# Kernel optimization log

Measured on AMD Instinct MI355X. Metric: run time of the kernel, lower is better.

## Reference

```python
import jax, jax.numpy as jnp
import numpy as np

N = 50000   # nodes
E = 800000  # edges (avg degree 16)
D = 128     # in_feats == out_feats


def setup_inputs() -> dict:
    key = jax.random.key(0)
    k1, k2, k3, k4 = jax.random.split(key, 4)
    h = jax.random.normal(k1, (N, D), dtype=jnp.float32)
    src = jax.random.randint(k2, (E,), 0, N, dtype=jnp.int32)
    dst = jax.random.randint(k3, (E,), 0, N, dtype=jnp.int32)
    snorm_n = jnp.ones((N, 1), dtype=jnp.float32)  # sqrt(1/N) replicated; identity-scaled here
    # NodeApply linear: Linear(2*D, D) with bias
    W = jax.random.normal(k4, (D, 2 * D), dtype=jnp.float32) / np.sqrt(2 * D).astype(np.float32)
    b = jnp.zeros((D,), dtype=jnp.float32)
    return {"h": h, "snorm_n": snorm_n, "W": W, "b": b, "src": src, "dst": dst}


def reference(h, snorm_n, W, b, src, dst):
    # dropout p=0.0 -> identity
    h_in = h
    # gather neighbor messages and segment-mean aggregate (MeanAggregator)
    ones = jnp.ones((src.shape[0],), dtype=h.dtype)
    deg = jax.ops.segment_sum(ones, dst, num_segments=N)            # [N]
    msg_sum = jax.ops.segment_sum(h[src], dst, num_segments=N)     # [N, D]
    c = msg_sum / jnp.maximum(deg, 1.0)[:, None]                   # zero-degree nodes -> c = 0
    # NodeApply: concat -> linear -> L2 normalize -> relu
    bundle = jnp.concatenate([h, c], axis=1) @ W.T + b             # [N, D]
    nrm = jnp.sqrt(jnp.sum(bundle * bundle, axis=1, keepdims=True))
    bundle = bundle / jnp.maximum(nrm, 1e-12)                      # F.normalize(p=2, dim=1)
    out = jax.nn.relu(bundle)
    # graph norm
    out = out * snorm_n
    # residual (in_feats == out_feats)
    return h_in + out
```

## Files before the change

### kernel.cpp

```cpp
#include <hip/hip_runtime.h>
#include <hip/hip_bf16.h>

#define TPB 256
#define CHUNK_LOG 13
#define CHUNK (1 << CHUNK_LOG)
#define HSTRIDE 12544

typedef __attribute__((ext_vector_type(8))) short bf16x8;
typedef __attribute__((ext_vector_type(4))) float f32x4;
typedef __attribute__((ext_vector_type(2))) float f32x2;

__device__ inline unsigned short f2bf(float f) {
    unsigned u = __float_as_uint(f);
    unsigned r = u + 0x7fffu + ((u >> 16) & 1u);
    return (unsigned short)(r >> 16);
}
__device__ inline float bf2f(unsigned short s) {
    return __uint_as_float(((unsigned)s) << 16);
}

__global__ void k_hist(const int* __restrict__ dst,
                       unsigned* __restrict__ hist32, unsigned char* __restrict__ lrank,
                       unsigned* ctr, int E) {
    __shared__ unsigned lhist[HSTRIDE];
    int b = blockIdx.x;
    if (b == 0 && threadIdx.x == 0) *ctr = 0u;
    for (int i = threadIdx.x; i < HSTRIDE; i += TPB) lhist[i] = 0;
    __syncthreads();
    int e0 = b << CHUNK_LOG;
    int e1 = min(e0 + CHUNK, E);
    for (int e = e0 + (int)threadIdx.x; e < e1; e += TPB) {
        int d = dst[e];
        unsigned sh = (d & 3) * 8;
        unsigned old = atomicAdd(&lhist[d >> 2], 1u << sh);
        lrank[e] = (unsigned char)((old >> sh) & 0xffu);
    }
    __syncthreads();
    for (int i = threadIdx.x; i < HSTRIDE; i += TPB)
        hist32[(size_t)b * HSTRIDE + i] = lhist[i];
}

__launch_bounds__(TPB)
__global__ void k_scan(const unsigned* __restrict__ hist32,
                       unsigned short* __restrict__ cbase,
                       int* __restrict__ bsum, unsigned* ctr,
                       int* __restrict__ offs, int N, int E, int NBH) {
    extern __shared__ unsigned tile[];
    __shared__ int sdata[4];
    __shared__ int sb[TPB];
    __shared__ int wsum[4];
    int NB = gridDim.x;
    int bid = blockIdx.x, tid = threadIdx.x;
    int lane = tid & 63, w = tid >> 6;

    int tileBase = bid * 64;
    int total = NBH * 64;
    for (int i = tid; i < total; i += TPB) {
        int b = i >> 6, c = i & 63;
        tile[i] = hist32[(size_t)b * HSTRIDE + tileBase + c];
    }
    __syncthreads();
    int n = bid * TPB + tid;
    unsigned sh = (tid & 3) * 8;
    int wcol = tid >> 2;
    int run = 0;
    for (int b = 0; b < NBH; ++b) {
        int c = (int)((tile[b * 64 + wcol] >> sh) & 0xffu);
        if (n < N) cbase[(size_t)b * N + n] = (unsigned short)run;
        run += c;
    }
    int dv = (n < N) ? run : 0;

    int s = dv;
    for (int o = 32; o; o >>= 1) s += __shfl_xor(s, o);
    if (lane == 0) sdata[w] = s;
    __syncthreads();
    if (tid == 0) {
        int tot = sdata[0] + sdata[1] + sdata[2] + sdata[3];
        __hip_atomic_store(&bsum[bid], tot, __ATOMIC_RELAXED, __HIP_MEMORY_SCOPE_AGENT);
        __hip_atomic_fetch_add(ctr, 1u, __ATOMIC_RELEASE, __HIP_MEMORY_SCOPE_AGENT);
        while (__hip_atomic_load(ctr, __ATOMIC_ACQUIRE, __HIP_MEMORY_SCOPE_AGENT)
               < (unsigned)NB)
            __builtin_amdgcn_s_sleep(2);
    }
    __syncthreads();

    int v = 0;
    if (tid < NB)
        v = __hip_atomic_load(&bsum[tid], __ATOMIC_RELAXED, __HIP_MEMORY_SCOPE_AGENT);
    int x = v;
    for (int o = 1; o < 64; o <<= 1) { int y = __shfl_up(x, o); if (lane >= o) x += y; }
    if (lane == 63) wsum[w] = x;
    __syncthreads();
    int add = 0;
    for (int k = 0; k < w; ++k) add += wsum[k];
    sb[tid] = add + x - v;
    __syncthreads();
    int base = sb[bid];

    int y2 = dv;
    for (int o = 1; o < 64; o <<= 1) { int z = __shfl_up(y2, o); if (lane >= o) y2 += z; }
    __syncthreads();
    if (lane == 63) wsum[w] = y2;
    __syncthreads();
    int add2 = 0;
    for (int k = 0; k < w; ++k) add2 += wsum[k];
    int ex = base + add2 + y2 - dv;
    if (n < N) offs[n] = ex;
    if (n == N - 1) offs[N] = E;
}

__global__ void k_scatterconv(const float* __restrict__ h, const float* __restrict__ W,
                              const int* __restrict__ src, const int* __restrict__ dst,
                              const unsigned char* __restrict__ lrank,
                              const unsigned short* __restrict__ cbase,
                              const int* __restrict__ offs,
                              unsigned short* __restrict__ esrc,
                              unsigned short* __restrict__ h_hi,
                              unsigned* __restrict__ h8,
                              unsigned short* __restrict__ Wb,
                              int N, int E, int nchunk) {
    int nh4 = N * 32;
    int totalc = nh4 + 8192;
    for (int t = blockIdx.x * TPB + threadIdx.x; t < totalc; t += gridDim.x * TPB) {
        if (t < nh4) {
            float4 v = ((const float4*)h)[t];
            ushort4 hi;
            hi.x = f2bf(v.x); hi.y = f2bf(v.y);
            hi.z = f2bf(v.z); hi.w = f2bf(v.w);
            ((ushort4*)h_hi)[t] = hi;
            int p8 = __builtin_amdgcn_cvt_pk_fp8_f32(v.x, v.y, 0, false);
            p8 = __builtin_amdgcn_cvt_pk_fp8_f32(v.z, v.w, p8, true);
            h8[t] = (unsigned)p8;
        } else {
            int w4 = t - nh4;
            float4 v = ((const float4*)W)[w4];
            ushort4 hi;
            hi.x = f2bf(v.x); hi.y = f2bf(v.y);
            hi.z = f2bf(v.z); hi.w = f2bf(v.w);
            ((ushort4*)Wb)[w4] = hi;
        }
    }
    int slice = blockIdx.x & 7;
    int chunk = blockIdx.x >> 3;
    int lo = (int)((long long)N * slice >> 3);
    int hi = (int)((long long)N * (slice + 1) >> 3);
    for (int e = chunk * TPB + threadIdx.x; e < E; e += nchunk * TPB) {
        int d = dst[e];
        if (d >= lo && d < hi) {
            int b = e >> CHUNK_LOG;
            int pos = offs[d] + (int)cbase[(size_t)b * N + d] + (int)lrank[e];
            esrc[pos] = (unsigned short)src[e];
        }
    }
}

#define AGG_ACC(u)                                                            \
    {                                                                         \
        f32x2 _p = __builtin_amdgcn_cvt_pk_f32_fp8((int)(u), false);          \
        f32x2 _q = __builtin_amdgcn_cvt_pk_f32_fp8((int)(u), true);           \
        a0 += _p.x; a1 += _p.y; a2 += _q.x; a3 += _q.y;                       \
    }

__global__ void k_agg(const unsigned* __restrict__ h8, const int* __restrict__ offs,
                      const unsigned short* __restrict__ esrc,
                      unsigned* __restrict__ c8, int N) {
    int wav = (blockIdx.x * TPB + threadIdx.x) >> 6;
    int half = (threadIdx.x >> 5) & 1;
    int hl = threadIdx.x & 31;
    int n = wav * 2 + half;
    if (n >= N) return;
    int beg = offs[n], end = offs[n + 1];
    int cnt = end - beg;
    float a0 = 0.f, a1 = 0.f, a2 = 0.f, a3 = 0.f;
    int e = beg;
    int s0 = 0, s1 = 0, s2 = 0, s3 = 0, s4 = 0, s5 = 0, s6 = 0, s7 = 0;
    if (cnt >= 8) {
        s0 = esrc[e];     s1 = esrc[e + 1]; s2 = esrc[e + 2]; s3 = esrc[e + 3];
        s4 = esrc[e + 4]; s5 = esrc[e + 5]; s6 = esrc[e + 6]; s7 = esrc[e + 7];
    }
    while (cnt >= 16) {
        int t0 = esrc[e + 8],  t1 = esrc[e + 9],  t2 = esrc[e + 10], t3 = esrc[e + 11];
        int t4 = esrc[e + 12], t5 = esrc[e + 13], t6 = esrc[e + 14], t7 = esrc[e + 15];
        unsigned u0 = h8[(size_t)s0 * 32 + hl];
        unsigned u1 = h8[(size_t)s1 * 32 + hl];
        unsigned u2 = h8[(size_t)s2 * 32 + hl];
        unsigned u3 = h8[(size_t)s3 * 32 + hl];
        unsigned u4 = h8[(size_t)s4 * 32 + hl];
        unsigned u5 = h8[(size_t)s5 * 32 + hl];
        unsigned u6 = h8[(size_t)s6 * 32 + hl];
        unsigned u7 = h8[(size_t)s7 * 32 + hl];
        AGG_ACC(u0) AGG_ACC(u1) AGG_ACC(u2) AGG_ACC(u3)
        AGG_ACC(u4) AGG_ACC(u5) AGG_ACC(u6) AGG_ACC(u7)
        s0 = t0; s1 = t1; s2 = t2; s3 = t3;
        s4 = t4; s5 = t5; s6 = t6; s7 = t7;
        e += 8; cnt -= 8;
    }
    if (cnt >= 8) {
        unsigned u0 = h8[(size_t)s0 * 32 + hl];
        unsigned u1 = h8[(size_t)s1 * 32 + hl];
        unsigned u2 = h8[(size_t)s2 * 32 + hl];
        unsigned u3 = h8[(size_t)s3 * 32 + hl];
        unsigned u4 = h8[(size_t)s4 * 32 + hl];
        unsigned u5 = h8[(size_t)s5 * 32 + hl];
        unsigned u6 = h8[(size_t)s6 * 32 + hl];
        unsigned u7 = h8[(size_t)s7 * 32 + hl];
        AGG_ACC(u0) AGG_ACC(u1) AGG_ACC(u2) AGG_ACC(u3)
        AGG_ACC(u4) AGG_ACC(u5) AGG_ACC(u6) AGG_ACC(u7)
        e += 8; cnt -= 8;
    }
    for (; cnt > 0; --cnt, ++e) {
        unsigned u0 = h8[(size_t)esrc[e] * 32 + hl];
        AGG_ACC(u0)
    }
    float inv = 1.0f / fmaxf((float)(end - beg), 1.0f);
    int pk = __builtin_amdgcn_cvt_pk_fp8_f32(a0 * inv, a1 * inv, 0, false);
    pk = __builtin_amdgcn_cvt_pk_fp8_f32(a2 * inv, a3 * inv, pk, true);
    c8[(size_t)n * 32 + hl] = (unsigned)pk;
}

__launch_bounds__(TPB)
__global__ void k_apply(const unsigned short* __restrict__ h_hi,
                        const unsigned char* __restrict__ c8,
                        const unsigned short* __restrict__ Wb,
                        const float* __restrict__ bia,
                        const float* __restrict__ snorm,
                        float* __restrict__ out, int N) {
    int lane = threadIdx.x & 63;
    int l15 = lane & 15, l4 = lane >> 4;
    int wave = threadIdx.x >> 6;
    int r0 = blockIdx.x * 128 + wave * 32;

    f32x4 acc[2][8] = {};

    #pragma unroll
    for (int kc = 0; kc < 8; ++kc) {
        bf16x8 Bf[8];
        #pragma unroll
        for (int n = 0; n < 8; ++n) {
            Bf[n] = *(const bf16x8*)((const char*)Wb +
                     ((size_t)(n * 16 + l15) * 512 + (size_t)kc * 64 + (size_t)l4 * 16));
        }
        #pragma unroll
        for (int rf = 0; rf < 2; ++rf) {
            int row = r0 + rf * 16 + l15;
            if (row > N - 1) row = N - 1;
            bf16x8 av;
            if (kc < 4) {
                av = *(const bf16x8*)((const char*)h_hi +
                      ((size_t)row * 256 + (size_t)kc * 64 + (size_t)l4 * 16));
            } else {
                uint2 cu = *(const uint2*)(c8 + (size_t)row * 128 +
                            (size_t)(kc - 4) * 32 + (size_t)l4 * 8);
                f32x2 p = __builtin_amdgcn_cvt_pk_f32_fp8((int)cu.x, false);
                f32x2 q = __builtin_amdgcn_cvt_pk_f32_fp8((int)cu.x, true);
                f32x2 r = __builtin_amdgcn_cvt_pk_f32_fp8((int)cu.y, false);
                f32x2 s = __builtin_amdgcn_cvt_pk_f32_fp8((int)cu.y, true);
                union { unsigned u[4]; bf16x8 v; } cv;
                asm("v_cvt_pk_bf16_f32 %0, %1, %2" : "=v"(cv.u[0]) : "v"(p.x), "v"(p.y));
                asm("v_cvt_pk_bf16_f32 %0, %1, %2" : "=v"(cv.u[1]) : "v"(q.x), "v"(q.y));
                asm("v_cvt_pk_bf16_f32 %0, %1, %2" : "=v"(cv.u[2]) : "v"(r.x), "v"(r.y));
                asm("v_cvt_pk_bf16_f32 %0, %1, %2" : "=v"(cv.u[3]) : "v"(s.x), "v"(s.y));
                av = cv.v;
            }
            #pragma unroll
            for (int n = 0; n < 8; ++n)
                acc[rf][n] = __builtin_amdgcn_mfma_f32_16x16x32_bf16(av, Bf[n], acc[rf][n], 0, 0, 0);
        }
    }

    float bn[8];
    #pragma unroll
    for (int n = 0; n < 8; ++n) bn[n] = bia[n * 16 + l15];

    #pragma unroll
    for (int rf = 0; rf < 2; ++rf) {
        float sq[4] = {0.f, 0.f, 0.f, 0.f};
        #pragma unroll
        for (int n = 0; n < 8; ++n) {
            #pragma unroll
            for (int g = 0; g < 4; ++g) {
                acc[rf][n][g] += bn[n];
                sq[g] += acc[rf][n][g] * acc[rf][n][g];
            }
        }
        #pragma unroll
        for (int g = 0; g < 4; ++g) {
            sq[g] += __shfl_xor(sq[g], 1);
            sq[g] += __shfl_xor(sq[g], 2);
            sq[g] += __shfl_xor(sq[g], 4);
            sq[g] += __shfl_xor(sq[g], 8);
        }
        #pragma unroll
        for (int g = 0; g < 4; ++g) {
            int row = r0 + rf * 16 + l4 * 4 + g;
            if (row < N) {
                float invn = 1.0f / fmaxf(sqrtf(sq[g]), 1e-12f);
                float sn = snorm[row];
                #pragma unroll
                for (int n = 0; n < 8; ++n) {
                    int col = n * 16 + l15;
                    float res = bf2f(h_hi[(size_t)row * 128 + col]);
                    float v = fmaxf(acc[rf][n][g] * invn, 0.f) * sn + res;
                    __builtin_nontemporal_store(v, &out[(size_t)row * 128 + col]);
                }
            }
        }
    }
}

extern "C" void kernel_launch(void* const* d_in, const int* in_sizes, int n_in,
                              void* d_out, int out_size, void* d_ws, size_t ws_size,
                              hipStream_t stream) {
    const float* h     = (const float*)d_in[0];
    const float* snorm = (const float*)d_in[1];
    const float* W     = (const float*)d_in[2];
    const float* b     = (const float*)d_in[3];
    const int*   src   = (const int*)d_in[4];
    const int*   dst   = (const int*)d_in[5];
    int N = in_sizes[1];
    int E = in_sizes[4];
    float* out = (float*)d_out;

    char* ws = (char*)d_ws;
    size_t off = 0;
    auto alloc = [&](size_t bytes) {
        void* ptr = ws + off;
        off = (off + bytes + 255) & ~(size_t)255;
        return ptr;
    };
    int NB  = (N + TPB - 1) / TPB;
    int NBH = (E + CHUNK - 1) >> CHUNK_LOG;
    int* offs   = (int*)alloc((size_t)(N + 1) * 4);
    int* bsum   = (int*)alloc((size_t)NB * 4);
    unsigned* ctr          = (unsigned*)alloc(256);
    unsigned* hist32       = (unsigned*)alloc((size_t)NBH * HSTRIDE * 4);
    unsigned short* cbase  = (unsigned short*)alloc((size_t)NBH * N * 2);
    unsigned char*  lrank  = (unsigned char*)alloc((size_t)E);
    unsigned short* esrc   = (unsigned short*)alloc((size_t)E * 2);
    unsigned short* h_hi   = (unsigned short*)alloc((size_t)N * 128 * 2);
    unsigned*       h8     = (unsigned*)alloc((size_t)N * 128);
    unsigned short* Wb     = (unsigned short*)alloc((size_t)128 * 256 * 2);
    unsigned* c8 = hist32;

    k_hist<<<NBH, TPB, 0, stream>>>(dst, hist32, lrank, ctr, E);

    size_t tile_bytes = (size_t)NBH * 64 * 4;
    k_scan<<<NB, TPB, tile_bytes, stream>>>(hist32, cbase, bsum, ctr, offs, N, E, NBH);

    int nchunk = 512;
    k_scatterconv<<<8 * nchunk, TPB, 0, stream>>>(h, W, src, dst, lrank, cbase, offs,
                                                  esrc, h_hi, h8, Wb, N, E, nchunk);

    int aggblk = (N + 7) / 8;
    k_agg<<<aggblk, TPB, 0, stream>>>(h8, offs, esrc, c8, N);

    int nblk = (N + 127) / 128;
    k_apply<<<nblk, TPB, 0, stream>>>(h_hi, (const unsigned char*)c8, Wb, b, snorm, out, N);
}
```

Measured before the change: 102.4 us.

## Slice fp8 features into column slabs and aggregate one slice per wave

```diff
diff --git a/kernel.cpp b/kernel.cpp
--- a/kernel.cpp
+++ b/kernel.cpp
@@ -117,7 +117,7 @@
                               const int* __restrict__ offs,
                               unsigned short* __restrict__ esrc,
                               unsigned short* __restrict__ h_hi,
-                              unsigned* __restrict__ h8,
+                              char* __restrict__ h8s,
                               unsigned short* __restrict__ Wb,
                               int N, int E, int nchunk) {
     int nh4 = N * 32;
@@ -131,7 +131,11 @@
             ((ushort4*)h_hi)[t] = hi;
             int p8 = __builtin_amdgcn_cvt_pk_fp8_f32(v.x, v.y, 0, false);
             p8 = __builtin_amdgcn_cvt_pk_fp8_f32(v.z, v.w, p8, true);
-            h8[t] = (unsigned)p8;
+            int row = t >> 5;
+            int k4 = (t & 31) << 2;
+            int sl = k4 >> 4;
+            int ko = k4 & 15;
+            *(unsigned*)(h8s + ((size_t)sl * N + row) * 16 + ko) = (unsigned)p8;
         } else {
             int w4 = t - nh4;
             float4 v = ((const float4*)W)[w4];
@@ -155,73 +159,46 @@
     }
 }
 
-#define AGG_ACC(u)                                                            \
-    {                                                                         \
-        f32x2 _p = __builtin_amdgcn_cvt_pk_f32_fp8((int)(u), false);          \
-        f32x2 _q = __builtin_amdgcn_cvt_pk_f32_fp8((int)(u), true);           \
-        a0 += _p.x; a1 += _p.y; a2 += _q.x; a3 += _q.y;                       \
-    }
-
-__global__ void k_agg(const unsigned* __restrict__ h8, const int* __restrict__ offs,
+__global__ void k_agg(const char* __restrict__ h8s, const int* __restrict__ offs,
                       const unsigned short* __restrict__ esrc,
-                      unsigned* __restrict__ c8, int N) {
-    int wav = (blockIdx.x * TPB + threadIdx.x) >> 6;
-    int half = (threadIdx.x >> 5) & 1;
-    int hl = threadIdx.x & 31;
-    int n = wav * 2 + half;
+                      char* __restrict__ c8s, int N) {
+    int slice = blockIdx.x & 7;
+    int wave = threadIdx.x >> 6;
+    int lane = threadIdx.x & 63;
+    int eg = lane >> 2, cl = lane & 3;
+    int n = (blockIdx.x >> 3) * 4 + wave;
     if (n >= N) return;
+    const char* hb = h8s + (size_t)slice * N * 16;
     int beg = offs[n], end = offs[n + 1];
-    int cnt = end - beg;
     float a0 = 0.f, a1 = 0.f, a2 = 0.f, a3 = 0.f;
-    int e = beg;
-    int s0 = 0, s1 = 0, s2 = 0, s3 = 0, s4 = 0, s5 = 0, s6 = 0, s7 = 0;
-    if (cnt >= 8) {
-        s0 = esrc[e];     s1 = esrc[e + 1]; s2 = esrc[e + 2]; s3 = esrc[e + 3];
-        s4 = esrc[e + 4]; s5 = esrc[e + 5]; s6 = esrc[e + 6]; s7 = esrc[e + 7];
-    }
-    while (cnt >= 16) {
-        int t0 = esrc[e + 8],  t1 = esrc[e + 9],  t2 = esrc[e + 10], t3 = esrc[e + 11];
-        int t4 = esrc[e + 12], t5 = esrc[e + 13], t6 = esrc[e + 14], t7 = esrc[e + 15];
-        unsigned u0 = h8[(size_t)s0 * 32 + hl];
-        unsigned u1 = h8[(size_t)s1 * 32 + hl];
-        unsigned u2 = h8[(size_t)s2 * 32 + hl];
-        unsigned u3 = h8[(size_t)s3 * 32 + hl];
-        unsigned u4 = h8[(size_t)s4 * 32 + hl];
-        unsigned u5 = h8[(size_t)s5 * 32 + hl];
-        unsigned u6 = h8[(size_t)s6 * 32 + hl];
-        unsigned u7 = h8[(size_t)s7 * 32 + hl];
-        AGG_ACC(u0) AGG_ACC(u1) AGG_ACC(u2) AGG_ACC(u3)
-        AGG_ACC(u4) AGG_ACC(u5) AGG_ACC(u6) AGG_ACC(u7)
-        s0 = t0; s1 = t1; s2 = t2; s3 = t3;
-        s4 = t4; s5 = t5; s6 = t6; s7 = t7;
-        e += 8; cnt -= 8;
-    }
-    if (cnt >= 8) {
-        unsigned u0 = h8[(size_t)s0 * 32 + hl];
-        unsigned u1 = h8[(size_t)s1 * 32 + hl];
-        unsigned u2 = h8[(size_t)s2 * 32 + hl];
-        unsigned u3 = h8[(size_t)s3 * 32 + hl];
-        unsigned u4 = h8[(size_t)s4 * 32 + hl];
-        unsigned u5 = h8[(size_t)s5 * 32 + hl];
-        unsigned u6 = h8[(size_t)s6 * 32 + hl];
-        unsigned u7 = h8[(size_t)s7 * 32 + hl];
-        AGG_ACC(u0) AGG_ACC(u1) AGG_ACC(u2) AGG_ACC(u3)
-        AGG_ACC(u4) AGG_ACC(u5) AGG_ACC(u6) AGG_ACC(u7)
-        e += 8; cnt -= 8;
-    }
-    for (; cnt > 0; --cnt, ++e) {
-        unsigned u0 = h8[(size_t)esrc[e] * 32 + hl];
-        AGG_ACC(u0)
-    }
-    float inv = 1.0f / fmaxf((float)(end - beg), 1.0f);
-    int pk = __builtin_amdgcn_cvt_pk_fp8_f32(a0 * inv, a1 * inv, 0, false);
-    pk = __builtin_amdgcn_cvt_pk_fp8_f32(a2 * inv, a3 * inv, pk, true);
-    c8[(size_t)n * 32 + hl] = (unsigned)pk;
+    for (int base = beg; base < end; base += 16) {
+        int e = base + eg;
+        unsigned u = 0;
+        if (e < end) {
+            int s = esrc[e];
+            u = *(const unsigned*)(hb + (size_t)s * 16 + cl * 4);
+        }
+        f32x2 p = __builtin_amdgcn_cvt_pk_f32_fp8((int)u, false);
+        f32x2 q = __builtin_amdgcn_cvt_pk_f32_fp8((int)u, true);
+        a0 += p.x; a1 += p.y; a2 += q.x; a3 += q.y;
+    }
+    for (int o = 4; o <= 32; o <<= 1) {
+        a0 += __shfl_xor(a0, o);
+        a1 += __shfl_xor(a1, o);
+        a2 += __shfl_xor(a2, o);
+        a3 += __shfl_xor(a3, o);
+    }
+    if (eg == 0) {
+        float inv = 1.0f / fmaxf((float)(end - beg), 1.0f);
+        int pk = __builtin_amdgcn_cvt_pk_fp8_f32(a0 * inv, a1 * inv, 0, false);
+        pk = __builtin_amdgcn_cvt_pk_fp8_f32(a2 * inv, a3 * inv, pk, true);
+        *(unsigned*)(c8s + ((size_t)slice * N + n) * 16 + cl * 4) = (unsigned)pk;
+    }
 }
 
 __launch_bounds__(TPB)
 __global__ void k_apply(const unsigned short* __restrict__ h_hi,
-                        const unsigned char* __restrict__ c8,
+                        const char* __restrict__ c8s,
                         const unsigned short* __restrict__ Wb,
                         const float* __restrict__ bia,
                         const float* __restrict__ snorm,
@@ -250,8 +227,10 @@
                 av = *(const bf16x8*)((const char*)h_hi +
                       ((size_t)row * 256 + (size_t)kc * 64 + (size_t)l4 * 16));
             } else {
-                uint2 cu = *(const uint2*)(c8 + (size_t)row * 128 +
-                            (size_t)(kc - 4) * 32 + (size_t)l4 * 8);
+                int off = (kc - 4) * 32 + l4 * 8;
+                int sl = off >> 4;
+                int ko = off & 15;
+                uint2 cu = *(const uint2*)(c8s + ((size_t)sl * N + row) * 16 + ko);
                 f32x2 p = __builtin_amdgcn_cvt_pk_f32_fp8((int)cu.x, false);
                 f32x2 q = __builtin_amdgcn_cvt_pk_f32_fp8((int)cu.x, true);
                 f32x2 r = __builtin_amdgcn_cvt_pk_f32_fp8((int)cu.y, false);
@@ -339,9 +318,9 @@
     unsigned char*  lrank  = (unsigned char*)alloc((size_t)E);
     unsigned short* esrc   = (unsigned short*)alloc((size_t)E * 2);
     unsigned short* h_hi   = (unsigned short*)alloc((size_t)N * 128 * 2);
-    unsigned*       h8     = (unsigned*)alloc((size_t)N * 128);
+    char*           h8s    = (char*)alloc((size_t)N * 128);
     unsigned short* Wb     = (unsigned short*)alloc((size_t)128 * 256 * 2);
-    unsigned* c8 = hist32;
+    char* c8s = (char*)hist32;
 
     k_hist<<<NBH, TPB, 0, stream>>>(dst, hist32, lrank, ctr, E);
 
@@ -350,11 +329,11 @@
 
     int nchunk = 512;
     k_scatterconv<<<8 * nchunk, TPB, 0, stream>>>(h, W, src, dst, lrank, cbase, offs,
-                                                  esrc, h_hi, h8, Wb, N, E, nchunk);
-
-    int aggblk = (N + 7) / 8;
-    k_agg<<<aggblk, TPB, 0, stream>>>(h8, offs, esrc, c8, N);
+                                                  esrc, h_hi, h8s, Wb, N, E, nchunk);
+
+    int aggblk = 8 * ((N + 3) / 4);
+    k_agg<<<aggblk, TPB, 0, stream>>>(h8s, offs, esrc, c8s, N);
 
     int nblk = (N + 127) / 128;
-    k_apply<<<nblk, TPB, 0, stream>>>(h_hi, (const unsigned char*)c8, Wb, b, snorm, out, N);
-}
+    k_apply<<<nblk, TPB, 0, stream>>>(h_hi, c8s, Wb, b, snorm, out, N);
+}
```

Result: slower. 168.6 us (+64.6%).
